# Performance work log

Measured on AMD Instinct MI355X. Metric: run time of the kernel, lower is better.

## Reference

```python
import jax, jax.numpy as jnp
import numpy as np

S = 512       # number of rnn_output rows (source positions)
T = 512       # number of target rows (queries)
DU = 512      # dim_u
DT = 512      # dim_target
D = DU + DT   # concat dim


def setup_inputs() -> dict:
    key = jax.random.key(0)
    k1, k2, k3, k4, k5, k6 = jax.random.split(key, 6)
    return {
        "rnn_outputs": jax.random.normal(k1, (S, DU), dtype=jnp.float32),
        "target": jax.random.normal(k2, (T, DT), dtype=jnp.float32),
        # nn.Linear(D, D): weight [D, D], bias [D]
        "W_lin": jax.random.normal(k3, (D, D), dtype=jnp.float32) * 0.02,
        "b_lin": jax.random.normal(k4, (D,), dtype=jnp.float32) * 0.02,
        # nn.Linear(D, 1): weight [1, D] stored flat, bias scalar
        "w_score": jax.random.normal(k5, (D,), dtype=jnp.float32) * 0.02,
        "b_score": jax.random.normal(k6, (), dtype=jnp.float32) * 0.02,
    }


def reference(rnn_outputs, target, W_lin, b_lin, w_score, b_score):
    du = rnn_outputs.shape[1]
    # linear(concat([rnn, tgt])) == rnn @ W[:, :du].T + tgt @ W[:, du:].T + b
    # (split the weight instead of materializing the [T, S, D] concat)
    A = rnn_outputs @ W_lin[:, :du].T            # [S, D]
    B = target @ W_lin[:, du:].T + b_lin         # [T, D]
    h = jnp.tanh(B[:, None, :] + A[None, :, :])  # [T, S, D]
    scores = h @ w_score + b_score               # [T, S]
    weights = jax.nn.softmax(scores, axis=1)     # softmax over source dim S
    # stack of per-row weighted sums == weights @ rnn_outputs
    return weights @ rnn_outputs                 # [T, dim_u]
```

## Files before the change

### kernel.cpp

```cpp
#include <hip/hip_runtime.h>


#define C2F 2.8853900817779268f

__global__ __launch_bounds__(256, 4) void k1_gemm_ab(
    const float* __restrict__ rnn, const float* __restrict__ tgt,
    const float* __restrict__ W, const float* __restrict__ bl,
    float* __restrict__ Abuf, float* __restrict__ Bbuf, int ksplit, int doexp)
{
    __shared__ float xt[32][68];
    __shared__ float wt[32][68];
    const int j0 = blockIdx.x * 64;
    const int i0 = blockIdx.y * 64;
    const int kz = blockIdx.z;
    const int klen = 512 / ksplit;
    const int kbase = kz * klen;
    const bool isB = (i0 >= 512);
    const float* __restrict__ in = isB ? tgt : rnn;
    const int irow0 = isB ? (i0 - 512) : i0;
    const int koff = isB ? 512 : 0;
    const int tid = threadIdx.x;
    const int lrow = tid >> 2;
    const int kq   = tid & 3;
    const int ti   = tid >> 4;
    const int tj   = tid & 15;
    const float* __restrict__ inp = in + (size_t)(irow0 + lrow) * 512 + kbase + kq * 8;
    const float* __restrict__ wp  = W  + (size_t)(j0 + lrow) * 1024 + koff + kbase + kq * 8;
    float acc[4][4] = {};
    float4 x0 = *(const float4*)(inp);
    float4 x1 = *(const float4*)(inp + 4);
    float4 w0 = *(const float4*)(wp);
    float4 w1 = *(const float4*)(wp + 4);
    for (int k0 = 0; k0 < klen; k0 += 32) {
        __syncthreads();
        xt[kq*8+0][lrow] = x0.x; xt[kq*8+1][lrow] = x0.y; xt[kq*8+2][lrow] = x0.z; xt[kq*8+3][lrow] = x0.w;
        xt[kq*8+4][lrow] = x1.x; xt[kq*8+5][lrow] = x1.y; xt[kq*8+6][lrow] = x1.z; xt[kq*8+7][lrow] = x1.w;
        wt[kq*8+0][lrow] = w0.x; wt[kq*8+1][lrow] = w0.y; wt[kq*8+2][lrow] = w0.z; wt[kq*8+3][lrow] = w0.w;
        wt[kq*8+4][lrow] = w1.x; wt[kq*8+5][lrow] = w1.y; wt[kq*8+6][lrow] = w1.z; wt[kq*8+7][lrow] = w1.w;
        __syncthreads();
        if (k0 + 32 < klen) {
            x0 = *(const float4*)(inp + k0 + 32);
            x1 = *(const float4*)(inp + k0 + 36);
            w0 = *(const float4*)(wp + k0 + 32);
            w1 = *(const float4*)(wp + k0 + 36);
        }
        #pragma unroll
        for (int k = 0; k < 32; ++k) {
            const float4 av = *(const float4*)&xt[k][ti * 4];
            const float4 bv = *(const float4*)&wt[k][tj * 4];
            const float ar[4] = {av.x, av.y, av.z, av.w};
            const float br[4] = {bv.x, bv.y, bv.z, bv.w};
            #pragma unroll
            for (int r = 0; r < 4; ++r)
                #pragma unroll
                for (int c = 0; c < 4; ++c)
                    acc[r][c] = __builtin_fmaf(ar[r], br[c], acc[r][c]);
        }
    }
    float4 bq = make_float4(0.f, 0.f, 0.f, 0.f);
    if (isB && kz == ksplit - 1) bq = *(const float4*)(bl + j0 + tj * 4);
    float* __restrict__ dst = (isB ? Bbuf : Abuf) + (size_t)kz * 524288;
    #pragma unroll
    for (int r = 0; r < 4; ++r) {
        float4 o;
        o.x = (acc[r][0] + bq.x) * C2F;
        o.y = (acc[r][1] + bq.y) * C2F;
        o.z = (acc[r][2] + bq.z) * C2F;
        o.w = (acc[r][3] + bq.w) * C2F;
        if (doexp) {
            o.x = __builtin_amdgcn_exp2f(o.x);
            o.y = __builtin_amdgcn_exp2f(o.y);
            o.z = __builtin_amdgcn_exp2f(o.z);
            o.w = __builtin_amdgcn_exp2f(o.w);
        }
        *(float4*)(dst + (size_t)(irow0 + ti * 4 + r) * 1024 + j0 + tj * 4) = o;
    }
}

__global__ __launch_bounds__(256, 4) void k1b_sum(float* __restrict__ ws4)
{
    const int i = (blockIdx.x * 256 + threadIdx.x) * 4;
    const float4 a0 = *(const float4*)(ws4 + i);
    const float4 a1 = *(const float4*)(ws4 + 524288 + i);
    const float4 b0 = *(const float4*)(ws4 + 2 * 524288 + i);
    const float4 b1 = *(const float4*)(ws4 + 3 * 524288 + i);
    float4 a, b;
    a.x = __builtin_amdgcn_exp2f(a0.x + a1.x);
    a.y = __builtin_amdgcn_exp2f(a0.y + a1.y);
    a.z = __builtin_amdgcn_exp2f(a0.z + a1.z);
    a.w = __builtin_amdgcn_exp2f(a0.w + a1.w);
    b.x = __builtin_amdgcn_exp2f(b0.x + b1.x);
    b.y = __builtin_amdgcn_exp2f(b0.y + b1.y);
    b.z = __builtin_amdgcn_exp2f(b0.z + b1.z);
    b.w = __builtin_amdgcn_exp2f(b0.w + b1.w);
    *(float4*)(ws4 + i) = a;
    *(float4*)(ws4 + 2 * 524288 + i) = b;
}

#define K2CELL(ACC, CC, RR) do {                                         \
    const float e0_ = __builtin_fmaf(A0.CC, B0.RR, 1.f);                 \
    const float e1_ = __builtin_fmaf(A1.CC, B1.RR, 1.f);                 \
    const float e2_ = __builtin_fmaf(A2.CC, B2.RR, 1.f);                 \
    const float e3_ = __builtin_fmaf(A3.CC, B3.RR, 1.f);                 \
    const float l01_ = e0_ * e1_;                                        \
    const float l23_ = e2_ * e3_;                                        \
    const float n01_ = __builtin_fmaf(wa.x, e1_, wa.y * e0_);            \
    const float n23_ = __builtin_fmaf(wa.z, e3_, wa.w * e2_);            \
    const float N_ = __builtin_fmaf(n01_, l23_, n23_ * l01_);            \
    ACC = __builtin_fmaf(N_, __builtin_amdgcn_rcpf(l01_ * l23_), ACC);   \
} while (0)

__global__ __launch_bounds__(256, 4) void k2_scores(
    const float* __restrict__ EA, const float* __restrict__ EB,
    const float* __restrict__ wsc, float* __restrict__ P, int dchunk)
{
    __shared__ float at[32][68];
    __shared__ float bt[32][68];
    __shared__ float wl[128];
    const int s0 = blockIdx.x * 64;
    const int t0 = blockIdx.y * 64;
    const int dz = blockIdx.z * dchunk;
    const int tid = threadIdx.x;
    if (tid < dchunk) wl[tid] = wsc[dz + tid];
    const int srow = tid & 63;
    const int kq   = tid >> 6;
    const int ti   = tid >> 4;
    const int tj   = tid & 15;
    const float* __restrict__ Arow = EA + (size_t)(s0 + srow) * 1024 + dz + kq * 8;
    const float* __restrict__ Brow = EB + (size_t)(t0 + srow) * 1024 + dz + kq * 8;
    float4 acc0 = make_float4(0.f,0.f,0.f,0.f);
    float4 acc1 = make_float4(0.f,0.f,0.f,0.f);
    float4 acc2 = make_float4(0.f,0.f,0.f,0.f);
    float4 acc3 = make_float4(0.f,0.f,0.f,0.f);
    float4 pa0 = *(const float4*)(Arow);
    float4 pa1 = *(const float4*)(Arow + 4);
    float4 pb0 = *(const float4*)(Brow);
    float4 pb1 = *(const float4*)(Brow + 4);
    for (int d0 = 0; d0 < dchunk; d0 += 32) {
        __syncthreads();
        at[kq*8+0][srow] = pa0.x; at[kq*8+1][srow] = pa0.y; at[kq*8+2][srow] = pa0.z; at[kq*8+3][srow] = pa0.w;
        at[kq*8+4][srow] = pa1.x; at[kq*8+5][srow] = pa1.y; at[kq*8+6][srow] = pa1.z; at[kq*8+7][srow] = pa1.w;
        bt[kq*8+0][srow] = pb0.x; bt[kq*8+1][srow] = pb0.y; bt[kq*8+2][srow] = pb0.z; bt[kq*8+3][srow] = pb0.w;
        bt[kq*8+4][srow] = pb1.x; bt[kq*8+5][srow] = pb1.y; bt[kq*8+6][srow] = pb1.z; bt[kq*8+7][srow] = pb1.w;
        __syncthreads();
        if (d0 + 32 < dchunk) {
            pa0 = *(const float4*)(Arow + d0 + 32);
            pa1 = *(const float4*)(Arow + d0 + 36);
            pb0 = *(const float4*)(Brow + d0 + 32);
            pb1 = *(const float4*)(Brow + d0 + 36);
        }
        for (int dd = 0; dd < 32; dd += 4) {
            const float4 wa = *(const float4*)&wl[d0 + dd];
            const float4 A0 = *(const float4*)&at[dd + 0][tj * 4];
            const float4 A1 = *(const float4*)&at[dd + 1][tj * 4];
            const float4 A2 = *(const float4*)&at[dd + 2][tj * 4];
            const float4 A3 = *(const float4*)&at[dd + 3][tj * 4];
            const float4 B0 = *(const float4*)&bt[dd + 0][ti * 4];
            const float4 B1 = *(const float4*)&bt[dd + 1][ti * 4];
            const float4 B2 = *(const float4*)&bt[dd + 2][ti * 4];
            const float4 B3 = *(const float4*)&bt[dd + 3][ti * 4];
            K2CELL(acc0.x, x, x); K2CELL(acc0.y, y, x); K2CELL(acc0.z, z, x); K2CELL(acc0.w, w, x);
            K2CELL(acc1.x, x, y); K2CELL(acc1.y, y, y); K2CELL(acc1.z, z, y); K2CELL(acc1.w, w, y);
            K2CELL(acc2.x, x, z); K2CELL(acc2.y, y, z); K2CELL(acc2.z, z, z); K2CELL(acc2.w, w, z);
            K2CELL(acc3.x, x, w); K2CELL(acc3.y, y, w); K2CELL(acc3.z, z, w); K2CELL(acc3.w, w, w);
        }
    }
    float* __restrict__ Pz = P + (size_t)blockIdx.z * 512 * 512;
    *(float4*)(Pz + (size_t)(t0 + ti * 4 + 0) * 512 + s0 + tj * 4) = acc0;
    *(float4*)(Pz + (size_t)(t0 + ti * 4 + 1) * 512 + s0 + tj * 4) = acc1;
    *(float4*)(Pz + (size_t)(t0 + ti * 4 + 2) * 512 + s0 + tj * 4) = acc2;
    *(float4*)(Pz + (size_t)(t0 + ti * 4 + 3) * 512 + s0 + tj * 4) = acc3;
}

__global__ __launch_bounds__(256, 4) void k3_softmax(
    const float* __restrict__ P, float* __restrict__ wgt, int nz)
{
    __shared__ float wm[4];
    __shared__ float wsum[4];
    const int t = blockIdx.x;
    const int tid = threadIdx.x;
    const size_t base = (size_t)t * 512 + tid * 2;
    float sx = 0.f, sy = 0.f;
    for (int z = 0; z < nz; ++z) {
        const float2 p = *(const float2*)(P + base + (size_t)z * 262144);
        sx += p.x; sy += p.y;
    }
    const float x0 = -2.f * sx;
    const float x1 = -2.f * sy;
    float m = fmaxf(x0, x1);
    #pragma unroll
    for (int off = 32; off; off >>= 1) m = fmaxf(m, __shfl_xor(m, off));
    if ((tid & 63) == 0) wm[tid >> 6] = m;
    __syncthreads();
    m = fmaxf(fmaxf(wm[0], wm[1]), fmaxf(wm[2], wm[3]));
    const float L2E = 1.4426950408889634f;
    const float e0 = __builtin_amdgcn_exp2f((x0 - m) * L2E);
    const float e1 = __builtin_amdgcn_exp2f((x1 - m) * L2E);
    float s = e0 + e1;
    #pragma unroll
    for (int off = 32; off; off >>= 1) s += __shfl_xor(s, off);
    if ((tid & 63) == 0) wsum[tid >> 6] = s;
    __syncthreads();
    s = wsum[0] + wsum[1] + wsum[2] + wsum[3];
    const float inv = 1.0f / s;
    float2 o; o.x = e0 * inv; o.y = e1 * inv;
    *(float2*)(wgt + (size_t)t * 512 + tid * 2) = o;
}

__global__ __launch_bounds__(256, 4) void k4_out(
    const float* __restrict__ wgt, const float* __restrict__ rnn,
    float* __restrict__ P4)
{
    __shared__ float wtt[32][68];
    __shared__ float rn[32][68];
    const int d0g = blockIdx.x * 64;
    const int t0g = blockIdx.y * 64;
    const int z   = blockIdx.z;
    const int tid = threadIdx.x;
    const int trow = tid & 63;
    const int kq   = tid >> 6;
    const int srw  = tid & 31;
    const int cq   = tid >> 5;
    const int ti = tid >> 4, tj = tid & 15;
    float acc[4][4] = {};
    for (int sc = z * 64; sc < z * 64 + 64; sc += 32) {
        const float4 w0 = *(const float4*)(wgt + (size_t)(t0g + trow) * 512 + sc + kq * 8);
        const float4 w1 = *(const float4*)(wgt + (size_t)(t0g + trow) * 512 + sc + kq * 8 + 4);
        const float4 r0 = *(const float4*)(rnn + (size_t)(sc + srw) * 512 + d0g + cq * 8);
        const float4 r1 = *(const float4*)(rnn + (size_t)(sc + srw) * 512 + d0g + cq * 8 + 4);
        __syncthreads();
        wtt[kq*8+0][trow] = w0.x; wtt[kq*8+1][trow] = w0.y; wtt[kq*8+2][trow] = w0.z; wtt[kq*8+3][trow] = w0.w;
        wtt[kq*8+4][trow] = w1.x; wtt[kq*8+5][trow] = w1.y; wtt[kq*8+6][trow] = w1.z; wtt[kq*8+7][trow] = w1.w;
        *(float4*)&rn[srw][cq * 8]     = r0;
        *(float4*)&rn[srw][cq * 8 + 4] = r1;
        __syncthreads();
        #pragma unroll
        for (int s = 0; s < 32; ++s) {
            const float4 av = *(const float4*)&wtt[s][ti * 4];
            const float4 bv = *(const float4*)&rn[s][tj * 4];
            const float ar[4] = {av.x, av.y, av.z, av.w};
            const float bc[4] = {bv.x, bv.y, bv.z, bv.w};
            #pragma unroll
            for (int r = 0; r < 4; ++r)
                #pragma unroll
                for (int c = 0; c < 4; ++c)
                    acc[r][c] = __builtin_fmaf(ar[r], bc[c], acc[r][c]);
        }
    }
    float* __restrict__ Pz = P4 + (size_t)z * 262144;
    #pragma unroll
    for (int r = 0; r < 4; ++r) {
        float4 o;
        o.x = acc[r][0]; o.y = acc[r][1]; o.z = acc[r][2]; o.w = acc[r][3];
        *(float4*)(Pz + (size_t)(t0g + ti * 4 + r) * 512 + d0g + tj * 4) = o;
    }
}

__global__ __launch_bounds__(256, 4) void k5_reduce(
    const float* __restrict__ P4, float* __restrict__ out)
{
    const int i = (blockIdx.x * 256 + threadIdx.x) * 4;
    float4 a = *(const float4*)(P4 + i);
    #pragma unroll
    for (int z = 1; z < 8; ++z) {
        const float4 b = *(const float4*)(P4 + (size_t)z * 262144 + i);
        a.x += b.x; a.y += b.y; a.z += b.z; a.w += b.w;
    }
    *(float4*)(out + i) = a;
}

extern "C" void kernel_launch(void* const* d_in, const int* in_sizes, int n_in,
                              void* d_out, int out_size, void* d_ws, size_t ws_size,
                              hipStream_t stream) {
    const float* rnn = (const float*)d_in[0];
    const float* tgt = (const float*)d_in[1];
    const float* W   = (const float*)d_in[2];
    const float* bl  = (const float*)d_in[3];
    const float* wsc = (const float*)d_in[4];
    float* out = (float*)d_out;

    const int nz = 8;
    const int dchunk = 1024 / nz;
    float* ws = (float*)d_ws;

    const bool split = (ws_size >= 17825792u);

    if (split) {
        float* A   = ws;
        float* B   = ws + 2 * 524288;
        float* P   = ws + 4 * 524288;
        float* wgt = P + (size_t)nz * 262144;
        float* P4  = P;
        k1_gemm_ab<<<dim3(16, 16, 2), 256, 0, stream>>>(rnn, tgt, W, bl, A, B, 2, 0);
        k1b_sum   <<<512,             256, 0, stream>>>(ws);
        k2_scores <<<dim3(8, 8, nz),  256, 0, stream>>>(A, B, wsc, P, dchunk);
        k3_softmax<<<512,             256, 0, stream>>>(P, wgt, nz);
        k4_out    <<<dim3(8, 8, 8),   256, 0, stream>>>(wgt, rnn, P4);
        k5_reduce <<<256,             256, 0, stream>>>(P4, out);
    } else {
        float* A   = ws;
        float* B   = ws + 524288;
        float* P   = ws + 2 * 524288;
        float* wgt = P + (size_t)nz * 262144;
        float* P4  = P;
        k1_gemm_ab<<<dim3(16, 16, 1), 256, 0, stream>>>(rnn, tgt, W, bl, A, B, 1, 1);
        k2_scores <<<dim3(8, 8, nz),  256, 0, stream>>>(A, B, wsc, P, dchunk);
        k3_softmax<<<512,             256, 0, stream>>>(P, wgt, nz);
        k4_out    <<<dim3(8, 8, 8),   256, 0, stream>>>(wgt, rnn, P4);
        k5_reduce <<<256,             256, 0, stream>>>(P4, out);
    }
}
```

Baseline: 69.50 us.

## Compute projection GEMM with split-bf16 MFMA instead of FP32 FMA

Replaces the FP32 SIMT tile GEMM that computes the A and B projections with a kernel using bf16 MFMA 16x16x32 instructions. Each FP32 input is split into a high and a low bf16 part, and three MFMA products (hh, lh, hl) are summed to approximate FP32 accuracy. The operands are converted and staged through LDS, with the next tile's global loads issued early. Only the split-K path uses the new kernel. It trades some precision and extra conversion work for matrix-core throughput on a GEMM that is only part of the total runtime.

```diff
diff --git a/kernel.cpp b/kernel.cpp
--- a/kernel.cpp
+++ b/kernel.cpp
@@ -2,6 +2,117 @@
 
 
 #define C2F 2.8853900817779268f
+
+typedef __attribute__((ext_vector_type(8))) short short8;
+typedef __attribute__((ext_vector_type(4))) float f32x4;
+
+__device__ __forceinline__ unsigned short bf16_rne(float f) {
+    unsigned u = __builtin_bit_cast(unsigned, f);
+    unsigned r = (u + 0x7FFFu + ((u >> 16) & 1u)) >> 16;
+    return (unsigned short)r;
+}
+__device__ __forceinline__ float bf16_f(unsigned short h) {
+    unsigned u = ((unsigned)h) << 16;
+    return __builtin_bit_cast(float, u);
+}
+
+__global__ __launch_bounds__(256, 4) void k1_mfma(
+    const float* __restrict__ rnn, const float* __restrict__ tgt,
+    const float* __restrict__ W, const float* __restrict__ bl,
+    float* __restrict__ Abuf, float* __restrict__ Bbuf, int ksplit)
+{
+    __shared__ unsigned short Xh[64][40], Xl[64][40], Wh[64][40], Wl[64][40];
+    const int j0 = blockIdx.x * 64;
+    const int i0 = blockIdx.y * 64;
+    const int kz = blockIdx.z;
+    const int klen = 512 / ksplit;
+    const int kbase = kz * klen;
+    const bool isB = (i0 >= 512);
+    const float* __restrict__ X = isB ? tgt : rnn;
+    const int irow0 = isB ? (i0 - 512) : i0;
+    const int koff = isB ? 512 : 0;
+    const int tid = threadIdx.x;
+    const int lane = tid & 63;
+    const int wv = tid >> 6;
+    const int isub = (wv & 1) * 32;
+    const int jsub = (wv >> 1) * 32;
+    const int srow = tid >> 2;
+    const int skq  = tid & 3;
+    const float* __restrict__ xp = X + (size_t)(irow0 + srow) * 512 + kbase + skq * 8;
+    const float* __restrict__ wp = W + (size_t)(j0 + srow) * 1024 + koff + kbase + skq * 8;
+    const int frow = lane & 15;
+    const int fk   = (lane >> 4) * 8;
+    f32x4 acc00 = {0.f,0.f,0.f,0.f}, acc01 = {0.f,0.f,0.f,0.f};
+    f32x4 acc10 = {0.f,0.f,0.f,0.f}, acc11 = {0.f,0.f,0.f,0.f};
+    float4 xv0 = *(const float4*)(xp);
+    float4 xv1 = *(const float4*)(xp + 4);
+    float4 wv0 = *(const float4*)(wp);
+    float4 wv1 = *(const float4*)(wp + 4);
+    for (int k0 = 0; k0 < klen; k0 += 32) {
+        __syncthreads();
+        {
+            short8 xh8, xl8, wh8, wl8;
+            const float xf[8] = {xv0.x, xv0.y, xv0.z, xv0.w, xv1.x, xv1.y, xv1.z, xv1.w};
+            const float wf[8] = {wv0.x, wv0.y, wv0.z, wv0.w, wv1.x, wv1.y, wv1.z, wv1.w};
+            #pragma unroll
+            for (int e = 0; e < 8; ++e) {
+                const unsigned short xh = bf16_rne(xf[e]);
+                const unsigned short wh = bf16_rne(wf[e]);
+                xh8[e] = (short)xh;
+                wh8[e] = (short)wh;
+                xl8[e] = (short)bf16_rne(xf[e] - bf16_f(xh));
+                wl8[e] = (short)bf16_rne(wf[e] - bf16_f(wh));
+            }
+            *(short8*)&Xh[srow][skq * 8] = xh8;
+            *(short8*)&Xl[srow][skq * 8] = xl8;
+            *(short8*)&Wh[srow][skq * 8] = wh8;
+            *(short8*)&Wl[srow][skq * 8] = wl8;
+        }
+        __syncthreads();
+        if (k0 + 32 < klen) {
+            xv0 = *(const float4*)(xp + k0 + 32);
+            xv1 = *(const float4*)(xp + k0 + 36);
+            wv0 = *(const float4*)(wp + k0 + 32);
+            wv1 = *(const float4*)(wp + k0 + 36);
+        }
+        const short8 ah0 = *(const short8*)&Xh[isub + frow][fk];
+        const short8 ah1 = *(const short8*)&Xh[isub + 16 + frow][fk];
+        const short8 bh0 = *(const short8*)&Wh[jsub + frow][fk];
+        const short8 bh1 = *(const short8*)&Wh[jsub + 16 + frow][fk];
+        acc00 = __builtin_amdgcn_mfma_f32_16x16x32_bf16(ah0, bh0, acc00, 0, 0, 0);
+        acc01 = __builtin_amdgcn_mfma_f32_16x16x32_bf16(ah0, bh1, acc01, 0, 0, 0);
+        acc10 = __builtin_amdgcn_mfma_f32_16x16x32_bf16(ah1, bh0, acc10, 0, 0, 0);
+        acc11 = __builtin_amdgcn_mfma_f32_16x16x32_bf16(ah1, bh1, acc11, 0, 0, 0);
+        const short8 al0 = *(const short8*)&Xl[isub + frow][fk];
+        const short8 al1 = *(const short8*)&Xl[isub + 16 + frow][fk];
+        acc00 = __builtin_amdgcn_mfma_f32_16x16x32_bf16(al0, bh0, acc00, 0, 0, 0);
+        acc01 = __builtin_amdgcn_mfma_f32_16x16x32_bf16(al0, bh1, acc01, 0, 0, 0);
+        acc10 = __builtin_amdgcn_mfma_f32_16x16x32_bf16(al1, bh0, acc10, 0, 0, 0);
+        acc11 = __builtin_amdgcn_mfma_f32_16x16x32_bf16(al1, bh1, acc11, 0, 0, 0);
+        const short8 bl0 = *(const short8*)&Wl[jsub + frow][fk];
+        const short8 bl1 = *(const short8*)&Wl[jsub + 16 + frow][fk];
+        acc00 = __builtin_amdgcn_mfma_f32_16x16x32_bf16(ah0, bl0, acc00, 0, 0, 0);
+        acc01 = __builtin_amdgcn_mfma_f32_16x16x32_bf16(ah0, bl1, acc01, 0, 0, 0);
+        acc10 = __builtin_amdgcn_mfma_f32_16x16x32_bf16(ah1, bl0, acc10, 0, 0, 0);
+        acc11 = __builtin_amdgcn_mfma_f32_16x16x32_bf16(ah1, bl1, acc11, 0, 0, 0);
+    }
+    const int orow = (lane >> 4) * 4;
+    const int ocol = lane & 15;
+    float* __restrict__ dst = (isB ? Bbuf : Abuf) + (size_t)kz * 524288;
+    const bool addb = isB && (kz == ksplit - 1);
+#define K1ST(ACC, MT, NT) do {                                            \
+    const int jl = jsub + (NT)*16 + ocol;                                 \
+    const float bb = addb ? bl[j0 + jl] : 0.f;                            \
+    const int il = isub + (MT)*16 + orow;                                 \
+    float* p = dst + (size_t)(irow0 + il) * 1024 + j0 + jl;               \
+    p[0]    = (ACC[0] + bb) * C2F;                                        \
+    p[1024] = (ACC[1] + bb) * C2F;                                        \
+    p[2048] = (ACC[2] + bb) * C2F;                                        \
+    p[3072] = (ACC[3] + bb) * C2F;                                        \
+} while (0)
+    K1ST(acc00, 0, 0); K1ST(acc01, 0, 1); K1ST(acc10, 1, 0); K1ST(acc11, 1, 1);
+#undef K1ST
+}
 
 __global__ __launch_bounds__(256, 4) void k1_gemm_ab(
     const float* __restrict__ rnn, const float* __restrict__ tgt,
@@ -291,7 +402,7 @@
         float* P   = ws + 4 * 524288;
         float* wgt = P + (size_t)nz * 262144;
         float* P4  = P;
-        k1_gemm_ab<<<dim3(16, 16, 2), 256, 0, stream>>>(rnn, tgt, W, bl, A, B, 2, 0);
+        k1_mfma   <<<dim3(16, 16, 2), 256, 0, stream>>>(rnn, tgt, W, bl, A, B, 2);
         k1b_sum   <<<512,             256, 0, stream>>>(ws);
         k2_scores <<<dim3(8, 8, nz),  256, 0, stream>>>(A, B, wsc, P, dchunk);
         k3_softmax<<<512,             256, 0, stream>>>(P, wgt, nz);
```

Result: faster. 59.96 us (-13.7%).
